# Kernel optimization log

Measured on AMD Instinct MI355X. Metric: run time of the kernel, lower is better.

The kernel has to match this reference:

```python
import jax, jax.numpy as jnp
import numpy as np
import math

B, S, D, H = 4, 2048, 512, 8
HD = D // H  # head dim = 64

def setup_inputs() -> dict:
    key = jax.random.key(0)
    ks = jax.random.split(key, 12)
    inp = {
        'queries': jax.random.normal(ks[0], (B, S, D), jnp.float32),
        'keys': jax.random.normal(ks[1], (B, S, D), jnp.float32),
        'values': jax.random.normal(ks[2], (B, S, D), jnp.float32),
        'valid_lens': jax.random.randint(ks[3], (B,), 0, 2048, jnp.int32),
        'Wq': jax.random.normal(ks[4], (D, D), jnp.float32) / math.sqrt(D),
        'bq': jnp.zeros((D,), jnp.float32),
        'Wk': jax.random.normal(ks[5], (D, D), jnp.float32) / math.sqrt(D),
        'bk': jnp.zeros((D,), jnp.float32),
        'Wv': jax.random.normal(ks[6], (D, D), jnp.float32) / math.sqrt(D),
        'bv': jnp.zeros((D,), jnp.float32),
        'Wo': jax.random.normal(ks[7], (D, D), jnp.float32) / math.sqrt(D),
        'bo': jnp.zeros((D,), jnp.float32),
    }
    return inp

def reference(queries, keys, values, valid_lens, Wq, bq, Wk, bk, Wv, bv, Wo, bo):
    # project and split heads: [B,S,D] -> [B,H,S,HD]
    def split_heads(x):
        return x.reshape(B, S, H, HD).transpose(0, 2, 1, 3)
    q = split_heads(queries @ Wq + bq)
    k = split_heads(keys @ Wk + bk)
    v = split_heads(values @ Wv + bv)
    # scores [B,H,Sq,Sk]
    scores = jnp.einsum('bhqd,bhkd->bhqk', q, k) / math.sqrt(HD)
    # masked softmax: mask key positions >= valid_len with -1e6 (d2l semantics)
    mask = jnp.arange(S)[None, None, None, :] < valid_lens[:, None, None, None]
    scores = jnp.where(mask, scores, -1e6)
    attn = jax.nn.softmax(scores, axis=-1)
    out = jnp.einsum('bhqk,bhkd->bhqd', attn, v)  # [B,H,S,HD]
    out = out.transpose(0, 2, 1, 3).reshape(B, S, D)
    return out @ Wo + bo
```

## Files before the change

### kernel.cpp

```cpp
#include <hip/hip_runtime.h>
#include <hip/hip_bf16.h>

typedef _Float16 half8 __attribute__((ext_vector_type(8)));
typedef _Float16 half4 __attribute__((ext_vector_type(4)));
typedef _Float16 half2t __attribute__((ext_vector_type(2)));
typedef float floatx4 __attribute__((ext_vector_type(4)));
typedef float floatx16 __attribute__((ext_vector_type(16)));
typedef unsigned int uint2v __attribute__((ext_vector_type(2)));

#define LOG2E 1.44269504088896340736f

__device__ __forceinline__ half8 cvt8r(floatx4 a, floatx4 b) {
    half8 h;
    h[0] = (_Float16)a[0]; h[1] = (_Float16)a[1]; h[2] = (_Float16)a[2]; h[3] = (_Float16)a[3];
    h[4] = (_Float16)b[0]; h[5] = (_Float16)b[1]; h[6] = (_Float16)b[2]; h[7] = (_Float16)b[3];
    return h;
}

union H8U { half8 h; half2t v2[4]; uint2v u[2]; };

__global__ __launch_bounds__(256) void transpose_w_kernel(
        const float* __restrict__ Wq, const float* __restrict__ Wk,
        const float* __restrict__ Wv, const float* __restrict__ Wo,
        _Float16* __restrict__ out) {
    const float* W = (blockIdx.z == 0) ? Wq : (blockIdx.z == 1) ? Wk : (blockIdx.z == 2) ? Wv : Wo;
    _Float16* o = out + (size_t)blockIdx.z * 512 * 512;
    __shared__ __align__(16) _Float16 t[64][72];
    int r0 = blockIdx.x * 64, c0 = blockIdx.y * 64;
    int tid = threadIdx.x;
    for (int i = 0; i < 2; i++) {
        int f = i * 256 + tid;
        int row = f >> 3, seg = f & 7;
        const float* p = W + (size_t)(r0 + row) * 512 + c0 + seg * 8;
        *(half8*)&t[row][seg * 8] = cvt8r(*(const floatx4*)p, *(const floatx4*)(p + 4));
    }
    __syncthreads();
    for (int i = 0; i < 2; i++) {
        int f = i * 256 + tid;
        int crow = f >> 3, seg = f & 7;
        half8 hv;
        for (int j = 0; j < 8; j++) hv[j] = t[seg * 8 + j][crow];
        *(half8*)(o + (size_t)(c0 + crow) * 512 + r0 + seg * 8) = hv;
    }
}

__global__ __launch_bounds__(256) void gemm_qkv_kernel(
        const float* __restrict__ Xq, const float* __restrict__ Xk, const float* __restrict__ Xv,
        const _Float16* __restrict__ WTall,
        const float* __restrict__ bq, const float* __restrict__ bk, const float* __restrict__ bv,
        const int* __restrict__ vlens,
        _Float16* __restrict__ qo, _Float16* __restrict__ ko2, _Float16* __restrict__ vto) {
    int z = blockIdx.z;
    int mBase = blockIdx.x * 64, nBase = blockIdx.y * 128;

    if (z >= 1) {
        int b_ = mBase >> 11, s0 = mBase & 2047;
        int L = vlens[b_];
        if (s0 >= L && !(z == 2 && L == 0)) return;
    }

    const float* X = (z == 0) ? Xq : (z == 1) ? Xk : Xv;
    const _Float16* BT = WTall + (size_t)z * 512 * 512;
    const float* bias = (z == 0) ? bq : (z == 1) ? bk : bv;

    __shared__ __align__(16) _Float16 Asm[64][72];
    __shared__ __align__(16) _Float16 Bsm[128][72];

    int tid = threadIdx.x;
    int wave = tid >> 6, lane = tid & 63;
    int lrow = lane & 15, quad = lane >> 4;
    int mrow = wave * 16 + lrow;

    const floatx4 fz = {0.f, 0.f, 0.f, 0.f};
    floatx4 acc[8];
    for (int i = 0; i < 8; i++) acc[i] = fz;

    int arow[2], aseg[2], brow[4], bseg[4];
    for (int i = 0; i < 2; i++) { int f = i * 256 + tid; arow[i] = f >> 3; aseg[i] = f & 7; }
    for (int i = 0; i < 4; i++) { int f = i * 256 + tid; brow[i] = f >> 3; bseg[i] = f & 7; }

    floatx4 areg[2][2];
    half8 breg[4];
    for (int i = 0; i < 2; i++) {
        const float* pa = X + (size_t)(mBase + arow[i]) * 512 + aseg[i] * 8;
        areg[i][0] = *(const floatx4*)pa;
        areg[i][1] = *(const floatx4*)(pa + 4);
    }
    for (int i = 0; i < 4; i++)
        breg[i] = *(const half8*)(BT + (size_t)(nBase + brow[i]) * 512 + bseg[i] * 8);

    for (int kb = 0; kb < 512; kb += 64) {
        for (int i = 0; i < 2; i++) *(half8*)&Asm[arow[i]][aseg[i] * 8] = cvt8r(areg[i][0], areg[i][1]);
        for (int i = 0; i < 4; i++) *(half8*)&Bsm[brow[i]][bseg[i] * 8] = breg[i];
        __syncthreads();
        if (kb + 64 < 512) {
            int kn = kb + 64;
            for (int i = 0; i < 2; i++) {
                const float* pa = X + (size_t)(mBase + arow[i]) * 512 + kn + aseg[i] * 8;
                areg[i][0] = *(const floatx4*)pa;
                areg[i][1] = *(const floatx4*)(pa + 4);
            }
            for (int i = 0; i < 4; i++)
                breg[i] = *(const half8*)(BT + (size_t)(nBase + brow[i]) * 512 + kn + bseg[i] * 8);
        }
        for (int kc = 0; kc < 2; kc++) {
            int ko_ = kc * 32 + quad * 8;
            half8 a = *(const half8*)&Asm[mrow][ko_];
            for (int nt = 0; nt < 8; nt++) {
                half8 b = *(const half8*)&Bsm[nt * 16 + lrow][ko_];
                acc[nt] = __builtin_amdgcn_mfma_f32_16x16x32_f16(a, b, acc[nt], 0, 0, 0);
            }
        }
        __syncthreads();
    }

    if (z == 2) {
        for (int nt = 0; nt < 8; nt++) {
            int gc = nBase + nt * 16 + lrow;
            float bb = bias[gc];
            int h = gc >> 6, hd = gc & 63;
            int gr = mBase + wave * 16 + quad * 4;
            int b_ = gr >> 11, s = gr & 2047;
            half4 hv;
            for (int r = 0; r < 4; r++) hv[r] = (_Float16)(acc[nt][r] + bb);
            *(half4*)(vto + (((size_t)(b_ * 8 + h) * 64 + hd) * 2048 + s)) = hv;
        }
    } else {
        _Float16* out = (z == 0) ? qo : ko2;
        for (int nt = 0; nt < 8; nt++) {
            int gc = nBase + nt * 16 + lrow;
            float bb = bias[gc];
            int h = gc >> 6, hd = gc & 63;
            for (int r = 0; r < 4; r++) {
                int gr = mBase + wave * 16 + quad * 4 + r;
                int b_ = gr >> 11, s = gr & 2047;
                out[(((size_t)b_ * 8 + h) * 2048 + s) * 64 + hd] = (_Float16)(acc[nt][r] + bb);
            }
        }
    }
}

__global__ __launch_bounds__(256) void attn_kernel(
        const _Float16* __restrict__ qws, const _Float16* __restrict__ kws,
        const _Float16* __restrict__ vtws, const int* __restrict__ vlens,
        _Float16* __restrict__ aout) {
    int idx = blockIdx.x;
    int b = ((idx & 3) + (idx >> 8)) & 3;
    int h = (idx >> 2) & 7;
    int q0 = ((idx >> 5) & 31) * 64;
    int bh = b * 8 + h;
    int L = vlens[b];
    bool uni = (L == 0);
    int nkt = uni ? 32 : ((L + 63) >> 6);
    int nfull = uni ? 0 : (L >> 6);

    int tid = threadIdx.x;
    int wid = tid >> 6;
    int wq = wid & 1, ks = wid >> 1;
    int lane = tid & 63;
    int l31 = lane & 31, hi = lane >> 5;

    __shared__ __align__(16) _Float16 ksm[2][64 * 64];
    __shared__ __align__(16) _Float16 vtsm[2][64 * 64];

    const _Float16* kbase = kws + (size_t)bh * 2048 * 64;
    const _Float16* vtbase = vtws + (size_t)bh * 64 * 2048;

    half8 qf[4];
    {
        const _Float16* qrow = qws + ((size_t)bh * 2048 + q0 + wq * 32 + l31) * 64;
#pragma unroll
        for (int kc = 0; kc < 4; kc++) {
            qf[kc] = *(const half8*)(qrow + kc * 16 + hi * 8);
            qf[kc] = qf[kc] * (_Float16)(0.125f * LOG2E);
        }
    }

    floatx16 oacc0, oacc1;
#pragma unroll
    for (int i = 0; i < 16; i++) { oacc0[i] = 0.f; oacc1[i] = 0.f; }
    float rs = 0.f;

    int htid = tid & 127;
    int tt = tid >> 7;
    int seg = htid & 7;
    int trow = htid >> 3;
    int xr = (l31 & 15) << 3;
    char* ksmB = (char*)&ksm[tt][0];
    char* vsmB = (char*)&vtsm[tt][0];

    half8 kreg[4], vreg[4];
    if (tt < nkt) {
        const _Float16* kp = kbase + (size_t)tt * 4096;
        const _Float16* vp = vtbase + tt * 64;
#pragma unroll
        for (int i = 0; i < 4; i++) {
            int row = i * 16 + trow;
            kreg[i] = *(const half8*)(kp + row * 64 + seg * 8);
            vreg[i] = *(const half8*)(vp + (size_t)row * 2048 + seg * 8);
        }
    }

    for (int kt2 = 0; kt2 < nkt; kt2 += 2) {
        if (kt2 + tt < nkt) {
#pragma unroll
            for (int i = 0; i < 4; i++) {
                int row = i * 16 + trow;
                int wo = row * 128 + ((seg * 16) ^ ((row & 15) << 3));
                H8U kv, vv;
                kv.h = kreg[i]; vv.h = vreg[i];
                *(uint2v*)(ksmB + wo) = kv.u[0];
                *(uint2v*)(ksmB + (wo ^ 8)) = kv.u[1];
                *(uint2v*)(vsmB + wo) = vv.u[0];
                *(uint2v*)(vsmB + (wo ^ 8)) = vv.u[1];
            }
        }
        __syncthreads();
        int nxt = kt2 + 2 + tt;
        if (nxt < nkt) {
            const _Float16* kp = kbase + (size_t)nxt * 4096;
            const _Float16* vp = vtbase + nxt * 64;
#pragma unroll
            for (int i = 0; i < 4; i++) {
                int row = i * 16 + trow;
                kreg[i] = *(const half8*)(kp + row * 64 + seg * 8);
                vreg[i] = *(const half8*)(vp + (size_t)row * 2048 + seg * 8);
            }
        }

        int kt = kt2 + ks;
        if (kt < nkt) {
#pragma unroll
            for (int t = 0; t < 2; t++) {
                floatx16 sacc;
#pragma unroll
                for (int i = 0; i < 16; i++) sacc[i] = 0.f;
                int rbase = (t * 32 + l31) * 128;
#pragma unroll
                for (int kc = 0; kc < 4; kc++) {
                    int off = rbase + ((kc * 32 + hi * 16) ^ xr);
                    H8U kf;
                    kf.u[0] = *(const uint2v*)(ksmB + off);
                    kf.u[1] = *(const uint2v*)(ksmB + (off ^ 8));
                    sacc = __builtin_amdgcn_mfma_f32_32x32x16_f16(kf.h, qf[kc], sacc, 0, 0, 0);
                }

                float p[16];
                if (kt < nfull) {
#pragma unroll
                    for (int r = 0; r < 16; r++) p[r] = exp2f(sacc[r]);
                } else {
                    int kb0 = kt * 64 + t * 32 + 4 * hi;
#pragma unroll
                    for (int r = 0; r < 16; r++) {
                        int key = kb0 + (r & 3) + 8 * (r >> 2);
                        p[r] = uni ? 1.0f : ((key < L) ? exp2f(sacc[r]) : 0.0f);
                    }
                }
#pragma unroll
                for (int r = 0; r < 16; r++) rs += p[r];

#pragma unroll
                for (int s2 = 0; s2 < 2; s2++) {
                    int s = t * 2 + s2;
                    H8U pa;
#pragma unroll
                    for (int j = 0; j < 8; j++) pa.h[j] = (_Float16)p[s2 * 8 + j];
                    int cb = (s * 32 + hi * 8) ^ xr;
                    {
                        int off = l31 * 128 + cb;
                        H8U vf;
                        vf.u[0] = *(const uint2v*)(vsmB + off);
                        vf.u[1] = *(const uint2v*)(vsmB + (off ^ 16));
                        oacc0 = __builtin_amdgcn_mfma_f32_32x32x16_f16(pa.h, vf.h, oacc0, 0, 0, 0);
                    }
                    {
                        int off = (32 + l31) * 128 + cb;
                        H8U vf;
                        vf.u[0] = *(const uint2v*)(vsmB + off);
                        vf.u[1] = *(const uint2v*)(vsmB + (off ^ 16));
                        oacc1 = __builtin_amdgcn_mfma_f32_32x32x16_f16(pa.h, vf.h, oacc1, 0, 0, 0);
                    }
                }
            }
        }
        __syncthreads();
    }

    float* ocs = (float*)&ksm[0][0];
    float* rss = (float*)&vtsm[0][0];
    if (ks == 1) {
        int sb = wq * 2048;
        rss[wq * 64 + lane] = rs;
#pragma unroll
        for (int i = 0; i < 16; i++) ocs[sb + i * 64 + lane] = oacc0[i];
#pragma unroll
        for (int i = 0; i < 16; i++) ocs[sb + (16 + i) * 64 + lane] = oacc1[i];
    }
    __syncthreads();
    if (ks == 0) {
        int sb = wq * 2048;
        rs += rss[wq * 64 + lane];
#pragma unroll
        for (int i = 0; i < 16; i++) oacc0[i] += ocs[sb + i * 64 + lane];
#pragma unroll
        for (int i = 0; i < 16; i++) oacc1[i] += ocs[sb + (16 + i) * 64 + lane];

        float rstot = rs + __shfl_xor(rs, 32, 64);
        _Float16* outb = aout + ((size_t)b * 2048 + q0 + wq * 32) * 512 + h * 64;
#pragma unroll
        for (int r = 0; r < 16; r++) {
            int qi = (r & 3) + 8 * (r >> 2) + 4 * hi;
            float inv = 1.0f / __shfl(rstot, qi, 64);
            outb[(size_t)qi * 512 + l31] = (_Float16)(oacc0[r] * inv);
            outb[(size_t)qi * 512 + 32 + l31] = (_Float16)(oacc1[r] * inv);
        }
    }
}

__global__ __launch_bounds__(256) void gemm_out_kernel(
        const _Float16* __restrict__ A, const _Float16* __restrict__ BT,
        const float* __restrict__ bias, float* __restrict__ out) {
    __shared__ __align__(16) _Float16 Asm[64][72];
    __shared__ __align__(16) _Float16 Bsm[128][72];

    int tid = threadIdx.x;
    int wave = tid >> 6, lane = tid & 63;
    int lrow = lane & 15, quad = lane >> 4;
    int mBase = blockIdx.x * 64, nBase = blockIdx.y * 128;
    int mrow = wave * 16 + lrow;

    const floatx4 fz = {0.f, 0.f, 0.f, 0.f};
    floatx4 acc[8];
    for (int i = 0; i < 8; i++) acc[i] = fz;

    int arow[2], aseg[2], brow[4], bseg[4];
    for (int i = 0; i < 2; i++) { int f = i * 256 + tid; arow[i] = f >> 3; aseg[i] = f & 7; }
    for (int i = 0; i < 4; i++) { int f = i * 256 + tid; brow[i] = f >> 3; bseg[i] = f & 7; }

    half8 areg[2], breg[4];
    for (int i = 0; i < 2; i++)
        areg[i] = *(const half8*)(A + (size_t)(mBase + arow[i]) * 512 + aseg[i] * 8);
    for (int i = 0; i < 4; i++)
        breg[i] = *(const half8*)(BT + (size_t)(nBase + brow[i]) * 512 + bseg[i] * 8);

    for (int kb = 0; kb < 512; kb += 64) {
        for (int i = 0; i < 2; i++) *(half8*)&Asm[arow[i]][aseg[i] * 8] = areg[i];
        for (int i = 0; i < 4; i++) *(half8*)&Bsm[brow[i]][bseg[i] * 8] = breg[i];
        __syncthreads();
        if (kb + 64 < 512) {
            int kn = kb + 64;
            for (int i = 0; i < 2; i++)
                areg[i] = *(const half8*)(A + (size_t)(mBase + arow[i]) * 512 + kn + aseg[i] * 8);
            for (int i = 0; i < 4; i++)
                breg[i] = *(const half8*)(BT + (size_t)(nBase + brow[i]) * 512 + kn + bseg[i] * 8);
        }
        for (int kc = 0; kc < 2; kc++) {
            int ko_ = kc * 32 + quad * 8;
            half8 a = *(const half8*)&Asm[mrow][ko_];
            for (int nt = 0; nt < 8; nt++) {
                half8 b = *(const half8*)&Bsm[nt * 16 + lrow][ko_];
                acc[nt] = __builtin_amdgcn_mfma_f32_16x16x32_f16(a, b, acc[nt], 0, 0, 0);
            }
        }
        __syncthreads();
    }

    for (int nt = 0; nt < 8; nt++) {
        int gc = nBase + nt * 16 + lrow;
        float bb = bias[gc];
        for (int r = 0; r < 4; r++) {
            int gr = mBase + wave * 16 + quad * 4 + r;
            out[(size_t)gr * 512 + gc] = acc[nt][r] + bb;
        }
    }
}

extern "C" void kernel_launch(void* const* d_in, const int* in_sizes, int n_in,
                              void* d_out, int out_size, void* d_ws, size_t ws_size,
                              hipStream_t stream) {
    const float* Q  = (const float*)d_in[0];
    const float* K  = (const float*)d_in[1];
    const float* V  = (const float*)d_in[2];
    const int*   VL = (const int*)d_in[3];
    const float* Wq = (const float*)d_in[4];
    const float* bq = (const float*)d_in[5];
    const float* Wk = (const float*)d_in[6];
    const float* bk = (const float*)d_in[7];
    const float* Wv = (const float*)d_in[8];
    const float* bv = (const float*)d_in[9];
    const float* Wo = (const float*)d_in[10];
    const float* bo = (const float*)d_in[11];

    char* ws = (char*)d_ws;
    _Float16* WT   = (_Float16*)ws;
    _Float16* qws  = (_Float16*)(ws + (size_t)(2)  * 1024 * 1024);
    _Float16* kws  = (_Float16*)(ws + (size_t)(10) * 1024 * 1024);
    _Float16* aout = (_Float16*)(ws + (size_t)(18) * 1024 * 1024);
    _Float16* vtws = (_Float16*)(ws + (size_t)(26) * 1024 * 1024);

    transpose_w_kernel<<<dim3(8, 8, 4), 256, 0, stream>>>(Wq, Wk, Wv, Wo, WT);
    gemm_qkv_kernel<<<dim3(128, 4, 3), 256, 0, stream>>>(Q, K, V, WT, bq, bk, bv, VL, qws, kws, vtws);
    attn_kernel<<<dim3(1024, 1, 1), 256, 0, stream>>>(qws, kws, vtws, VL, aout);
    gemm_out_kernel<<<dim3(128, 4, 1), 256, 0, stream>>>(aout, WT + (size_t)3 * 512 * 512, bo, (float*)d_out);
}
```

Measured before the change: 192.6 us.

## Use persistent attention blocks with atomic work queue ordered by batch cost

The attention kernel becomes persistent, launching 512 blocks that pull (batch, head, q-tile) items from a global atomic counter. The counter is reset in the transpose kernel. Items are ordered so batches with longer valid lengths (more key tiles) are handed out first, which balances the uneven work caused by valid_lens. It also switches P-to-fp16 packing to the packed round-toward-zero convert. The costs are an atomic plus an extra barrier per item and slightly different rounding of P.

```diff
diff --git a/kernel.cpp b/kernel.cpp
--- a/kernel.cpp
+++ b/kernel.cpp
@@ -19,10 +19,15 @@
 
 union H8U { half8 h; half2t v2[4]; uint2v u[2]; };
 
+__device__ __forceinline__ half2t pk16(float a, float b) {
+    return __builtin_bit_cast(half2t, __builtin_amdgcn_cvt_pkrtz(a, b));
+}
+
 __global__ __launch_bounds__(256) void transpose_w_kernel(
         const float* __restrict__ Wq, const float* __restrict__ Wk,
         const float* __restrict__ Wv, const float* __restrict__ Wo,
-        _Float16* __restrict__ out) {
+        _Float16* __restrict__ out, int* __restrict__ ctr) {
+    if (blockIdx.x == 0 && blockIdx.y == 0 && blockIdx.z == 0 && threadIdx.x == 0) *ctr = 0;
     const float* W = (blockIdx.z == 0) ? Wq : (blockIdx.z == 1) ? Wk : (blockIdx.z == 2) ? Wv : Wo;
     _Float16* o = out + (size_t)blockIdx.z * 512 * 512;
     __shared__ __align__(16) _Float16 t[64][72];
@@ -143,17 +148,7 @@
 __global__ __launch_bounds__(256) void attn_kernel(
         const _Float16* __restrict__ qws, const _Float16* __restrict__ kws,
         const _Float16* __restrict__ vtws, const int* __restrict__ vlens,
-        _Float16* __restrict__ aout) {
-    int idx = blockIdx.x;
-    int b = ((idx & 3) + (idx >> 8)) & 3;
-    int h = (idx >> 2) & 7;
-    int q0 = ((idx >> 5) & 31) * 64;
-    int bh = b * 8 + h;
-    int L = vlens[b];
-    bool uni = (L == 0);
-    int nkt = uni ? 32 : ((L + 63) >> 6);
-    int nfull = uni ? 0 : (L >> 6);
-
+        _Float16* __restrict__ aout, int* __restrict__ ctr) {
     int tid = threadIdx.x;
     int wid = tid >> 6;
     int wq = wid & 1, ks = wid >> 1;
@@ -162,24 +157,20 @@
 
     __shared__ __align__(16) _Float16 ksm[2][64 * 64];
     __shared__ __align__(16) _Float16 vtsm[2][64 * 64];
-
-    const _Float16* kbase = kws + (size_t)bh * 2048 * 64;
-    const _Float16* vtbase = vtws + (size_t)bh * 64 * 2048;
-
-    half8 qf[4];
-    {
-        const _Float16* qrow = qws + ((size_t)bh * 2048 + q0 + wq * 32 + l31) * 64;
-#pragma unroll
-        for (int kc = 0; kc < 4; kc++) {
-            qf[kc] = *(const half8*)(qrow + kc * 16 + hi * 8);
-            qf[kc] = qf[kc] * (_Float16)(0.125f * LOG2E);
-        }
-    }
-
-    floatx16 oacc0, oacc1;
-#pragma unroll
-    for (int i = 0; i < 16; i++) { oacc0[i] = 0.f; oacc1[i] = 0.f; }
-    float rs = 0.f;
+    __shared__ int sm_item;
+
+    int Lb[4], cost[4];
+#pragma unroll
+    for (int i = 0; i < 4; i++) {
+        Lb[i] = vlens[i];
+        cost[i] = (Lb[i] == 0) ? 32 : ((Lb[i] + 63) >> 6);
+    }
+    int ord[4] = {0, 1, 2, 3};
+#pragma unroll
+    for (int i = 0; i < 3; i++)
+#pragma unroll
+        for (int j = 0; j < 3; j++)
+            if (cost[ord[j]] < cost[ord[j + 1]]) { int t_ = ord[j]; ord[j] = ord[j + 1]; ord[j + 1] = t_; }
 
     int htid = tid & 127;
     int tt = tid >> 7;
@@ -189,37 +180,44 @@
     char* ksmB = (char*)&ksm[tt][0];
     char* vsmB = (char*)&vtsm[tt][0];
 
-    half8 kreg[4], vreg[4];
-    if (tt < nkt) {
-        const _Float16* kp = kbase + (size_t)tt * 4096;
-        const _Float16* vp = vtbase + tt * 64;
-#pragma unroll
-        for (int i = 0; i < 4; i++) {
-            int row = i * 16 + trow;
-            kreg[i] = *(const half8*)(kp + row * 64 + seg * 8);
-            vreg[i] = *(const half8*)(vp + (size_t)row * 2048 + seg * 8);
-        }
-    }
-
-    for (int kt2 = 0; kt2 < nkt; kt2 += 2) {
-        if (kt2 + tt < nkt) {
-#pragma unroll
-            for (int i = 0; i < 4; i++) {
-                int row = i * 16 + trow;
-                int wo = row * 128 + ((seg * 16) ^ ((row & 15) << 3));
-                H8U kv, vv;
-                kv.h = kreg[i]; vv.h = vreg[i];
-                *(uint2v*)(ksmB + wo) = kv.u[0];
-                *(uint2v*)(ksmB + (wo ^ 8)) = kv.u[1];
-                *(uint2v*)(vsmB + wo) = vv.u[0];
-                *(uint2v*)(vsmB + (wo ^ 8)) = vv.u[1];
-            }
-        }
-        __syncthreads();
-        int nxt = kt2 + 2 + tt;
-        if (nxt < nkt) {
-            const _Float16* kp = kbase + (size_t)nxt * 4096;
-            const _Float16* vp = vtbase + nxt * 64;
+    while (true) {
+        if (tid == 0) sm_item = atomicAdd(ctr, 1);
+        __syncthreads();
+        int g = sm_item;
+        if (g >= 1024) break;
+
+        int b = ord[g >> 8];
+        int r_ = g & 255;
+        int h = r_ >> 5;
+        int q0 = (r_ & 31) * 64;
+        int bh = b * 8 + h;
+        int L = Lb[b];
+        bool uni = (L == 0);
+        int nkt = uni ? 32 : ((L + 63) >> 6);
+        int nfull = uni ? 0 : (L >> 6);
+
+        const _Float16* kbase = kws + (size_t)bh * 2048 * 64;
+        const _Float16* vtbase = vtws + (size_t)bh * 64 * 2048;
+
+        half8 qf[4];
+        {
+            const _Float16* qrow = qws + ((size_t)bh * 2048 + q0 + wq * 32 + l31) * 64;
+#pragma unroll
+            for (int kc = 0; kc < 4; kc++) {
+                qf[kc] = *(const half8*)(qrow + kc * 16 + hi * 8);
+                qf[kc] = qf[kc] * (_Float16)(0.125f * LOG2E);
+            }
+        }
+
+        floatx16 oacc0, oacc1;
+#pragma unroll
+        for (int i = 0; i < 16; i++) { oacc0[i] = 0.f; oacc1[i] = 0.f; }
+        float rs = 0.f;
+
+        half8 kreg[4], vreg[4];
+        if (tt < nkt) {
+            const _Float16* kp = kbase + (size_t)tt * 4096;
+            const _Float16* vp = vtbase + tt * 64;
 #pragma unroll
             for (int i = 0; i < 4; i++) {
                 int row = i * 16 + trow;
@@ -228,93 +226,123 @@
             }
         }
 
-        int kt = kt2 + ks;
-        if (kt < nkt) {
-#pragma unroll
-            for (int t = 0; t < 2; t++) {
-                floatx16 sacc;
-#pragma unroll
-                for (int i = 0; i < 16; i++) sacc[i] = 0.f;
-                int rbase = (t * 32 + l31) * 128;
-#pragma unroll
-                for (int kc = 0; kc < 4; kc++) {
-                    int off = rbase + ((kc * 32 + hi * 16) ^ xr);
-                    H8U kf;
-                    kf.u[0] = *(const uint2v*)(ksmB + off);
-                    kf.u[1] = *(const uint2v*)(ksmB + (off ^ 8));
-                    sacc = __builtin_amdgcn_mfma_f32_32x32x16_f16(kf.h, qf[kc], sacc, 0, 0, 0);
+        for (int kt2 = 0; kt2 < nkt; kt2 += 2) {
+            if (kt2 + tt < nkt) {
+#pragma unroll
+                for (int i = 0; i < 4; i++) {
+                    int row = i * 16 + trow;
+                    int wo = row * 128 + ((seg * 16) ^ ((row & 15) << 3));
+                    H8U kv, vv;
+                    kv.h = kreg[i]; vv.h = vreg[i];
+                    *(uint2v*)(ksmB + wo) = kv.u[0];
+                    *(uint2v*)(ksmB + (wo ^ 8)) = kv.u[1];
+                    *(uint2v*)(vsmB + wo) = vv.u[0];
+                    *(uint2v*)(vsmB + (wo ^ 8)) = vv.u[1];
                 }
-
-                float p[16];
-                if (kt < nfull) {
-#pragma unroll
-                    for (int r = 0; r < 16; r++) p[r] = exp2f(sacc[r]);
-                } else {
-                    int kb0 = kt * 64 + t * 32 + 4 * hi;
-#pragma unroll
-                    for (int r = 0; r < 16; r++) {
-                        int key = kb0 + (r & 3) + 8 * (r >> 2);
-                        p[r] = uni ? 1.0f : ((key < L) ? exp2f(sacc[r]) : 0.0f);
+            }
+            __syncthreads();
+            int nxt = kt2 + 2 + tt;
+            if (nxt < nkt) {
+                const _Float16* kp = kbase + (size_t)nxt * 4096;
+                const _Float16* vp = vtbase + nxt * 64;
+#pragma unroll
+                for (int i = 0; i < 4; i++) {
+                    int row = i * 16 + trow;
+                    kreg[i] = *(const half8*)(kp + row * 64 + seg * 8);
+                    vreg[i] = *(const half8*)(vp + (size_t)row * 2048 + seg * 8);
+                }
+            }
+
+            int kt = kt2 + ks;
+            if (kt < nkt) {
+#pragma unroll
+                for (int t = 0; t < 2; t++) {
+                    floatx16 sacc;
+#pragma unroll
+                    for (int i = 0; i < 16; i++) sacc[i] = 0.f;
+                    int rbase = (t * 32 + l31) * 128;
+#pragma unroll
+                    for (int kc = 0; kc < 4; kc++) {
+                        int off = rbase + ((kc * 32 + hi * 16) ^ xr);
+                        H8U kf;
+                        kf.u[0] = *(const uint2v*)(ksmB + off);
+                        kf.u[1] = *(const uint2v*)(ksmB + (off ^ 8));
+                        sacc = __builtin_amdgcn_mfma_f32_32x32x16_f16(kf.h, qf[kc], sacc, 0, 0, 0);
+                    }
+
+                    float p[16];
+                    if (kt < nfull) {
+#pragma unroll
+                        for (int r = 0; r < 16; r++) p[r] = exp2f(sacc[r]);
+                    } else {
+                        int kb0 = kt * 64 + t * 32 + 4 * hi;
+#pragma unroll
+                        for (int r = 0; r < 16; r++) {
+                            int key = kb0 + (r & 3) + 8 * (r >> 2);
+                            p[r] = uni ? 1.0f : ((key < L) ? exp2f(sacc[r]) : 0.0f);
+                        }
+                    }
+#pragma unroll
+                    for (int r = 0; r < 16; r++) rs += p[r];
+
+#pragma unroll
+                    for (int s2 = 0; s2 < 2; s2++) {
+                        int s = t * 2 + s2;
+                        H8U pa;
+#pragma unroll
+                        for (int jj = 0; jj < 4; jj++)
+                            pa.v2[jj] = pk16(p[s2 * 8 + jj * 2], p[s2 * 8 + jj * 2 + 1]);
+                        int cb = (s * 32 + hi * 8) ^ xr;
+                        {
+                            int off = l31 * 128 + cb;
+                            H8U vf;
+                            vf.u[0] = *(const uint2v*)(vsmB + off);
+                            vf.u[1] = *(const uint2v*)(vsmB + (off ^ 16));
+                            oacc0 = __builtin_amdgcn_mfma_f32_32x32x16_f16(pa.h, vf.h, oacc0, 0, 0, 0);
+                        }
+                        {
+                            int off = (32 + l31) * 128 + cb;
+                            H8U vf;
+                            vf.u[0] = *(const uint2v*)(vsmB + off);
+                            vf.u[1] = *(const uint2v*)(vsmB + (off ^ 16));
+                            oacc1 = __builtin_amdgcn_mfma_f32_32x32x16_f16(pa.h, vf.h, oacc1, 0, 0, 0);
+                        }
                     }
                 }
-#pragma unroll
-                for (int r = 0; r < 16; r++) rs += p[r];
-
-#pragma unroll
-                for (int s2 = 0; s2 < 2; s2++) {
-                    int s = t * 2 + s2;
-                    H8U pa;
-#pragma unroll
-                    for (int j = 0; j < 8; j++) pa.h[j] = (_Float16)p[s2 * 8 + j];
-                    int cb = (s * 32 + hi * 8) ^ xr;
-                    {
-                        int off = l31 * 128 + cb;
-                        H8U vf;
-                        vf.u[0] = *(const uint2v*)(vsmB + off);
-                        vf.u[1] = *(const uint2v*)(vsmB + (off ^ 16));
-                        oacc0 = __builtin_amdgcn_mfma_f32_32x32x16_f16(pa.h, vf.h, oacc0, 0, 0, 0);
-                    }
-                    {
-                        int off = (32 + l31) * 128 + cb;
-                        H8U vf;
-                        vf.u[0] = *(const uint2v*)(vsmB + off);
-                        vf.u[1] = *(const uint2v*)(vsmB + (off ^ 16));
-                        oacc1 = __builtin_amdgcn_mfma_f32_32x32x16_f16(pa.h, vf.h, oacc1, 0, 0, 0);
-                    }
-                }
-            }
-        }
-        __syncthreads();
-    }
-
-    float* ocs = (float*)&ksm[0][0];
-    float* rss = (float*)&vtsm[0][0];
-    if (ks == 1) {
-        int sb = wq * 2048;
-        rss[wq * 64 + lane] = rs;
-#pragma unroll
-        for (int i = 0; i < 16; i++) ocs[sb + i * 64 + lane] = oacc0[i];
-#pragma unroll
-        for (int i = 0; i < 16; i++) ocs[sb + (16 + i) * 64 + lane] = oacc1[i];
-    }
-    __syncthreads();
-    if (ks == 0) {
-        int sb = wq * 2048;
-        rs += rss[wq * 64 + lane];
-#pragma unroll
-        for (int i = 0; i < 16; i++) oacc0[i] += ocs[sb + i * 64 + lane];
-#pragma unroll
-        for (int i = 0; i < 16; i++) oacc1[i] += ocs[sb + (16 + i) * 64 + lane];
-
-        float rstot = rs + __shfl_xor(rs, 32, 64);
-        _Float16* outb = aout + ((size_t)b * 2048 + q0 + wq * 32) * 512 + h * 64;
-#pragma unroll
-        for (int r = 0; r < 16; r++) {
-            int qi = (r & 3) + 8 * (r >> 2) + 4 * hi;
-            float inv = 1.0f / __shfl(rstot, qi, 64);
-            outb[(size_t)qi * 512 + l31] = (_Float16)(oacc0[r] * inv);
-            outb[(size_t)qi * 512 + 32 + l31] = (_Float16)(oacc1[r] * inv);
-        }
+            }
+            __syncthreads();
+        }
+
+        float* ocs = (float*)&ksm[0][0];
+        float* rss = (float*)&vtsm[0][0];
+        if (ks == 1) {
+            int sb = wq * 2048;
+            rss[wq * 64 + lane] = rs;
+#pragma unroll
+            for (int i = 0; i < 16; i++) ocs[sb + i * 64 + lane] = oacc0[i];
+#pragma unroll
+            for (int i = 0; i < 16; i++) ocs[sb + (16 + i) * 64 + lane] = oacc1[i];
+        }
+        __syncthreads();
+        if (ks == 0) {
+            int sb = wq * 2048;
+            rs += rss[wq * 64 + lane];
+#pragma unroll
+            for (int i = 0; i < 16; i++) oacc0[i] += ocs[sb + i * 64 + lane];
+#pragma unroll
+            for (int i = 0; i < 16; i++) oacc1[i] += ocs[sb + (16 + i) * 64 + lane];
+
+            float rstot = rs + __shfl_xor(rs, 32, 64);
+            _Float16* outb = aout + ((size_t)b * 2048 + q0 + wq * 32) * 512 + h * 64;
+#pragma unroll
+            for (int r = 0; r < 16; r++) {
+                int qi = (r & 3) + 8 * (r >> 2) + 4 * hi;
+                float inv = 1.0f / __shfl(rstot, qi, 64);
+                outb[(size_t)qi * 512 + l31] = (_Float16)(oacc0[r] * inv);
+                outb[(size_t)qi * 512 + 32 + l31] = (_Float16)(oacc1[r] * inv);
+            }
+        }
+        __syncthreads();
     }
 }
 
@@ -398,9 +426,10 @@
     _Float16* kws  = (_Float16*)(ws + (size_t)(10) * 1024 * 1024);
     _Float16* aout = (_Float16*)(ws + (size_t)(18) * 1024 * 1024);
     _Float16* vtws = (_Float16*)(ws + (size_t)(26) * 1024 * 1024);
-
-    transpose_w_kernel<<<dim3(8, 8, 4), 256, 0, stream>>>(Wq, Wk, Wv, Wo, WT);
+    int*      ctr  = (int*)     (ws + (size_t)(34) * 1024 * 1024);
+
+    transpose_w_kernel<<<dim3(8, 8, 4), 256, 0, stream>>>(Wq, Wk, Wv, Wo, WT, ctr);
     gemm_qkv_kernel<<<dim3(128, 4, 3), 256, 0, stream>>>(Q, K, V, WT, bq, bk, bv, VL, qws, kws, vtws);
-    attn_kernel<<<dim3(1024, 1, 1), 256, 0, stream>>>(qws, kws, vtws, VL, aout);
+    attn_kernel<<<dim3(512, 1, 1), 256, 0, stream>>>(qws, kws, vtws, VL, aout, ctr);
     gemm_out_kernel<<<dim3(128, 4, 1), 256, 0, stream>>>(aout, WT + (size_t)3 * 512 * 512, bo, (float*)d_out);
 }
```

New measurement: 234.0 us. 1.21x slower.
